# Kernel optimization log

Hardware: AMD Instinct MI355X
Metric: run time of the kernel (lower is better)

The kernel has to match this reference:

```python
import jax, jax.numpy as jnp
import numpy as np

N_NODES = 100000
N_EDGES = 1600000
D_IN = 128
D_OUT = 128


def setup_inputs() -> dict:
    key = jax.random.key(0)
    ks = jax.random.split(key, 7)
    x = jax.random.normal(ks[0], (N_NODES, D_IN), dtype=jnp.float32)
    y = jax.random.normal(ks[1], (N_NODES, D_OUT), dtype=jnp.float32)
    edge_src = jax.random.randint(ks[2], (N_EDGES,), 0, N_NODES, dtype=jnp.int32)
    edge_dst = jax.random.randint(ks[3], (N_EDGES,), 0, N_NODES, dtype=jnp.int32)
    adj_vals = jax.random.uniform(ks[4], (N_EDGES,), dtype=jnp.float32)
    weight = jax.random.normal(ks[5], (D_IN, D_OUT), dtype=jnp.float32) * (1.0 / np.sqrt(D_IN))
    bias = jax.random.normal(ks[6], (D_OUT,), dtype=jnp.float32) * 0.01
    return {"x": x, "y": y, "edge_src": edge_src, "edge_dst": edge_dst,
            "adj_vals": adj_vals, "weight": weight, "bias": bias}


def reference(x, y, edge_src, edge_dst, adj_vals, weight, bias):
    # GraphConvolution: support = x @ W ; out = spmm(adj, support) + bias
    support = x @ weight                      # [N, d_out]
    msgs = support[edge_src] * adj_vals[:, None]   # [E, d_out] gather + scale
    agg = jax.ops.segment_sum(msgs, edge_dst, num_segments=N_NODES)  # [N, d_out]
    gc_out = agg + bias
    # ResGCN epilogue: relu(gc_out + y); dropout is identity in eval (p=0.0)
    return jax.nn.relu(gc_out + y)
```

## Files before the change

kernel.cpp:

```cpp
#include <hip/hip_runtime.h>

#define D 128
#define CE 8192
#define NB_MAX 1024
#define MAXC 512
#define EBUF 3072
#define CHUNK 1024
#define WTP 136


typedef __attribute__((ext_vector_type(8))) short bf16x8;
typedef __attribute__((ext_vector_type(4))) float f32x4;

__device__ __forceinline__ unsigned short f2bf(float f) {
  unsigned u = __float_as_uint(f);
  unsigned r = (u + 0x7fffu + ((u >> 16) & 1u)) >> 16;
  return (unsigned short)r;
}

__device__ __forceinline__ int wave_iscan(int v) {
  const int lane = threadIdx.x & 63;
#pragma unroll
  for (int off = 1; off < 64; off <<= 1) {
    int u = __shfl_up(v, off, 64);
    if (lane >= off) v += u;
  }
  return v;
}

__device__ __forceinline__ int seg_find(const int* pref, int nC, int i) {
  int lo = 0, hi = nC;
  while (hi - lo > 1) {
    int mid = (lo + hi) >> 1;
    if (pref[mid] <= i) lo = mid; else hi = mid;
  }
  return lo;
}

__global__ __launch_bounds__(256) void convert_kernel(
    const float4* __restrict__ x4, ushort4* __restrict__ xb4, int n4, int nxblk,
    const float* __restrict__ w, unsigned short* __restrict__ wt) {
  int bid = blockIdx.x;
  if (bid < nxblk) {
    int i = bid * 256 + threadIdx.x;
    if (i < n4) {
      float4 v = x4[i];
      ushort4 r;
      r.x = f2bf(v.x);
      r.y = f2bf(v.y);
      r.z = f2bf(v.z);
      r.w = f2bf(v.w);
      xb4[i] = r;
    }
  } else {
    int idx = (bid - nxblk) * 256 + threadIdx.x;
    int n = idx >> 7, k = idx & 127;
    wt[n * WTP + k] = f2bf(w[k * D + n]);
  }
}

__global__ __launch_bounds__(1024) void chunk_sort_kernel(
    const int* __restrict__ src, const int* __restrict__ dst,
    const float* __restrict__ adj, int2* __restrict__ edges,
    unsigned short* __restrict__ ofs, int nE, int nB) {
  __shared__ int2 stage[CE];
  __shared__ int h[NB_MAX + 4];
  __shared__ int wsum[16];
  const int t = threadIdx.x;
  const int c = blockIdx.x;
  const int e0 = c * CE;
  const int n = min(CE, nE - e0);
  const int lane = t & 63, wid = t >> 6;

  for (int i = t; i < NB_MAX + 4; i += 1024) h[i] = 0;
  __syncthreads();

  int dreg[8];
#pragma unroll
  for (int k = 0; k < 8; ++k) {
    int i = k * 1024 + t;
    if (i < n) {
      int d = dst[e0 + i];
      dreg[k] = d;
      atomicAdd(&h[d >> 7], 1);
    }
  }
  __syncthreads();

  int v = h[t];
  int inc = wave_iscan(v);
  if (lane == 63) wsum[wid] = inc;
  __syncthreads();
  if (wid == 0) {
    int p = (lane < 16) ? wsum[lane] : 0;
    int pi = wave_iscan(p);
    if (lane < 16) wsum[lane] = pi;
  }
  __syncthreads();
  h[t] = inc - v + (wid ? wsum[wid - 1] : 0);
  __syncthreads();

  unsigned short* o = ofs + (size_t)c * (nB + 1);
  for (int i = t; i <= nB; i += 1024)
    o[i] = (unsigned short)(i < NB_MAX ? h[i] : n);
  __syncthreads();

#pragma unroll
  for (int k = 0; k < 8; ++k) {
    int i = k * 1024 + t;
    if (i < n) {
      int d = dreg[k];
      int pos = atomicAdd(&h[d >> 7], 1);
      int2 ev;
      ev.x = src[e0 + i] | ((d & 127) << 17);
      ev.y = __float_as_int(adj[e0 + i]);
      stage[pos] = ev;
    }
  }
  __syncthreads();

  for (int i = t; i < n; i += 1024) edges[e0 + i] = stage[i];
}

__global__ __launch_bounds__(256) void bucket_gather_kernel(
    const int2* __restrict__ tmp, const unsigned short* __restrict__ ofs,
    const uint2* __restrict__ xb, char* out, int nC, int nB, int nNodes) {
  __shared__ int2 ebuf[EBUF];
  __shared__ int segst[MAXC];
  __shared__ int pref[MAXC + 1];
  __shared__ int cnt[128];
  __shared__ int cur[128];
  __shared__ int sstart[128];
  __shared__ int w4[4];
  const int t = threadIdx.x;
  const int b = blockIdx.x;
  const int lane = t & 63, wid = t >> 6;

  const int c0 = 2 * t, c1 = 2 * t + 1;
  int n0 = 0, n1 = 0;
  if (c0 < nC) {
    int s0 = ofs[(size_t)c0 * (nB + 1) + b];
    int s1 = ofs[(size_t)c0 * (nB + 1) + b + 1];
    segst[c0] = c0 * CE + s0;
    n0 = s1 - s0;
  }
  if (c1 < nC) {
    int s0 = ofs[(size_t)c1 * (nB + 1) + b];
    int s1 = ofs[(size_t)c1 * (nB + 1) + b + 1];
    segst[c1] = c1 * CE + s0;
    n1 = s1 - s0;
  }
  int tt = n0 + n1;
  int inc = wave_iscan(tt);
  if (lane == 63) w4[wid] = inc;
  __syncthreads();
  int add = 0;
  for (int i = 0; i < wid; ++i) add += w4[i];
  int incl = inc + add;
  int excl = incl - tt;
  if (c0 < nC) pref[c0] = excl;
  if (c1 < nC) pref[c1] = excl + n0;
  if (t == 255) pref[nC] = incl;
  __syncthreads();
  const int m = pref[nC];

  const int gi = t >> 5;
  const int q = t & 31;
  float4 acc[16];
#pragma unroll
  for (int k = 0; k < 16; ++k) acc[k] = make_float4(0.f, 0.f, 0.f, 0.f);

  for (int w0 = 0; w0 < m; w0 += EBUF) {
    const int w1 = min(m, w0 + EBUF);
    if (t < 128) cnt[t] = 0;
    __syncthreads();

    for (int i = w0 + t; i < w1; i += 256) {
      int lo = seg_find(pref, nC, i);
      int sx = ((const int*)tmp)[(size_t)(segst[lo] + (i - pref[lo])) * 2];
      atomicAdd(&cnt[(sx >> 17) & 127], 1);
    }
    __syncthreads();

    int cv = (t < 128) ? cnt[t] : 0;
    int cinc = wave_iscan(cv);
    if (t == 63) w4[0] = cinc;
    __syncthreads();
    int cst = cinc - cv + ((t >= 64 && t < 128) ? w4[0] : 0);
    if (t < 128) {
      sstart[t] = cst;
      cur[t] = cst;
    }
    __syncthreads();

    for (int i = w0 + t; i < w1; i += 256) {
      int lo = seg_find(pref, nC, i);
      int2 ev = tmp[segst[lo] + (i - pref[lo])];
      int pos = atomicAdd(&cur[(ev.x >> 17) & 127], 1);
      ebuf[pos] = ev;
    }
    __syncthreads();

#pragma unroll
    for (int k = 0; k < 16; ++k) {
      const int dl = gi * 16 + k;
      int j = sstart[dl];
      const int e = cur[dl];
      for (; j + 3 < e; j += 4) {
        int2 e0 = ebuf[j], e1 = ebuf[j + 1], e2 = ebuf[j + 2], e3 = ebuf[j + 3];
        float a0 = __int_as_float(e0.y), a1 = __int_as_float(e1.y);
        float a2 = __int_as_float(e2.y), a3 = __int_as_float(e3.y);
        uint2 v0 = xb[(size_t)(e0.x & 0x1FFFF) * 32 + q];
        uint2 v1 = xb[(size_t)(e1.x & 0x1FFFF) * 32 + q];
        uint2 v2 = xb[(size_t)(e2.x & 0x1FFFF) * 32 + q];
        uint2 v3 = xb[(size_t)(e3.x & 0x1FFFF) * 32 + q];
        acc[k].x = fmaf(a0, __uint_as_float(v0.x << 16), acc[k].x);
        acc[k].y = fmaf(a0, __uint_as_float(v0.x & 0xffff0000u), acc[k].y);
        acc[k].z = fmaf(a0, __uint_as_float(v0.y << 16), acc[k].z);
        acc[k].w = fmaf(a0, __uint_as_float(v0.y & 0xffff0000u), acc[k].w);
        acc[k].x = fmaf(a1, __uint_as_float(v1.x << 16), acc[k].x);
        acc[k].y = fmaf(a1, __uint_as_float(v1.x & 0xffff0000u), acc[k].y);
        acc[k].z = fmaf(a1, __uint_as_float(v1.y << 16), acc[k].z);
        acc[k].w = fmaf(a1, __uint_as_float(v1.y & 0xffff0000u), acc[k].w);
        acc[k].x = fmaf(a2, __uint_as_float(v2.x << 16), acc[k].x);
        acc[k].y = fmaf(a2, __uint_as_float(v2.x & 0xffff0000u), acc[k].y);
        acc[k].z = fmaf(a2, __uint_as_float(v2.y << 16), acc[k].z);
        acc[k].w = fmaf(a2, __uint_as_float(v2.y & 0xffff0000u), acc[k].w);
        acc[k].x = fmaf(a3, __uint_as_float(v3.x << 16), acc[k].x);
        acc[k].y = fmaf(a3, __uint_as_float(v3.x & 0xffff0000u), acc[k].y);
        acc[k].z = fmaf(a3, __uint_as_float(v3.y << 16), acc[k].z);
        acc[k].w = fmaf(a3, __uint_as_float(v3.y & 0xffff0000u), acc[k].w);
      }
      for (; j < e; ++j) {
        int2 e0 = ebuf[j];
        float a0 = __int_as_float(e0.y);
        uint2 v0 = xb[(size_t)(e0.x & 0x1FFFF) * 32 + q];
        acc[k].x = fmaf(a0, __uint_as_float(v0.x << 16), acc[k].x);
        acc[k].y = fmaf(a0, __uint_as_float(v0.x & 0xffff0000u), acc[k].y);
        acc[k].z = fmaf(a0, __uint_as_float(v0.y << 16), acc[k].z);
        acc[k].w = fmaf(a0, __uint_as_float(v0.y & 0xffff0000u), acc[k].w);
      }
    }
    __syncthreads();
  }

#pragma unroll
  for (int k = 0; k < 16; ++k) {
    int g = b * 128 + gi * 16 + k;
    if (g < nNodes) {
      uint2 pk;
      pk.x = (unsigned)f2bf(acc[k].x) | ((unsigned)f2bf(acc[k].y) << 16);
      pk.y = (unsigned)f2bf(acc[k].z) | ((unsigned)f2bf(acc[k].w) << 16);
      ((uint2*)(out + (size_t)g * 512))[q] = pk;
    }
  }
}

__global__ __launch_bounds__(256) void gemm_mfma_kernel(
    const char* aggb, const unsigned short* __restrict__ wt,
    const float* __restrict__ y, const float* __restrict__ bias,
    float* out, int nNodes) {
  __shared__ unsigned short sWt[D * WTP];
  const int t = threadIdx.x;
  for (int i = t; i < D * WTP / 8; i += 256)
    ((int4*)sWt)[i] = ((const int4*)wt)[i];
  __syncthreads();

  const int w = t >> 6, l = t & 63;
  const int quad = l >> 4, m = l & 15;
  const int row0 = blockIdx.x * 128 + w * 32;

  const int ar0 = min(row0 + m, nNodes - 1);
  const int ar1 = min(row0 + 16 + m, nNodes - 1);
  const char* pa0 = aggb + (size_t)ar0 * 512;
  const char* pa1 = aggb + (size_t)ar1 * 512;

  f32x4 acc0[8], acc1[8];
#pragma unroll
  for (int nt = 0; nt < 8; ++nt) {
    acc0[nt] = (f32x4){0.f, 0.f, 0.f, 0.f};
    acc1[nt] = (f32x4){0.f, 0.f, 0.f, 0.f};
  }

#pragma unroll
  for (int ks = 0; ks < 4; ++ks) {
    const int kof = ks * 32 + quad * 8;
    bf16x8 a0 = *(const bf16x8*)(pa0 + kof * 2);
    bf16x8 a1 = *(const bf16x8*)(pa1 + kof * 2);
#pragma unroll
    for (int nt = 0; nt < 8; ++nt) {
      bf16x8 b = *(const bf16x8*)&sWt[(nt * 16 + m) * WTP + kof];
      acc0[nt] = __builtin_amdgcn_mfma_f32_16x16x32_bf16(a0, b, acc0[nt], 0, 0, 0);
      acc1[nt] = __builtin_amdgcn_mfma_f32_16x16x32_bf16(a1, b, acc1[nt], 0, 0, 0);
    }
  }

  float bv[8];
#pragma unroll
  for (int nt = 0; nt < 8; ++nt) bv[nt] = bias[nt * 16 + m];

#pragma unroll
  for (int s = 0; s < 2; ++s) {
#pragma unroll
    for (int r = 0; r < 4; ++r) {
      int row = row0 + s * 16 + quad * 4 + r;
      if (row >= nNodes) continue;
      const float* yr = y + (size_t)row * D;
      float* orow = out + (size_t)row * D;
#pragma unroll
      for (int nt = 0; nt < 8; ++nt) {
        int c = nt * 16 + m;
        float v = (s == 0 ? acc0[nt][r] : acc1[nt][r]) + yr[c] + bv[nt];
        orow[c] = fmaxf(v, 0.f);
      }
    }
  }
}

__global__ __launch_bounds__(256) void zero_counts_kernel(int* __restrict__ c, int n) {
  int i = blockIdx.x * 256 + threadIdx.x;
  if (i < n) c[i] = 0;
}

__global__ __launch_bounds__(256) void hist_kernel(
    const int* __restrict__ dst, int* __restrict__ counts, int nE) {
  int e = blockIdx.x * 256 + threadIdx.x;
  if (e < nE) atomicAdd(&counts[dst[e]], 1);
}

__global__ __launch_bounds__(256) void scan_partial_kernel(
    const int* __restrict__ counts, int* __restrict__ chunk_sum, int n) {
  __shared__ int sdata[256];
  int b = blockIdx.x, t = threadIdx.x;
  int base = b * CHUNK + t * 4;
  int s = 0;
#pragma unroll
  for (int k = 0; k < 4; ++k) {
    int i = base + k;
    if (i < n) s += counts[i];
  }
  sdata[t] = s;
  __syncthreads();
  for (int off = 128; off > 0; off >>= 1) {
    if (t < off) sdata[t] += sdata[t + off];
    __syncthreads();
  }
  if (t == 0) chunk_sum[b] = sdata[0];
}

__global__ void scan_chunks_kernel(const int* __restrict__ chunk_sum,
                                   int* __restrict__ chunk_off,
                                   int* __restrict__ row_start, int nchunks, int n) {
  if (threadIdx.x == 0 && blockIdx.x == 0) {
    int run = 0;
    for (int i = 0; i < nchunks; ++i) {
      chunk_off[i] = run;
      run += chunk_sum[i];
    }
    row_start[n] = run;
  }
}

__global__ __launch_bounds__(256) void scan_final_kernel(
    const int* __restrict__ counts, const int* __restrict__ chunk_off,
    int* __restrict__ row_start, int* __restrict__ cursor, int n) {
  __shared__ int sdata[256];
  int b = blockIdx.x, t = threadIdx.x;
  int base = b * CHUNK + t * 4;
  int c[4] = {0, 0, 0, 0};
#pragma unroll
  for (int k = 0; k < 4; ++k) {
    int i = base + k;
    if (i < n) c[k] = counts[i];
  }
  int tsum = c[0] + c[1] + c[2] + c[3];
  sdata[t] = tsum;
  __syncthreads();
  for (int off = 1; off < 256; off <<= 1) {
    int v = (t >= off) ? sdata[t - off] : 0;
    __syncthreads();
    sdata[t] += v;
    __syncthreads();
  }
  int run = sdata[t] - tsum + chunk_off[b];
#pragma unroll
  for (int k = 0; k < 4; ++k) {
    int i = base + k;
    if (i < n) {
      row_start[i] = run;
      cursor[i] = run;
      run += c[k];
    }
  }
}

__global__ __launch_bounds__(256) void scatter_sort_kernel(
    const int* __restrict__ src, const int* __restrict__ dst,
    const float* __restrict__ adj, int* __restrict__ cursor,
    int2* __restrict__ edges, int nE) {
  int e = blockIdx.x * 256 + threadIdx.x;
  if (e >= nE) return;
  int d = dst[e];
  int2 ev;
  ev.x = src[e];
  ev.y = __float_as_int(adj[e]);
  int pos = atomicAdd(&cursor[d], 1);
  edges[pos] = ev;
}

__global__ __launch_bounds__(256) void gather_fp32_kernel(
    const float* __restrict__ x, const int* __restrict__ row_start,
    const int2* __restrict__ edges, float* __restrict__ out, int nNodes) {
  int g = (blockIdx.x * 256 + threadIdx.x) >> 5;
  int q = threadIdx.x & 31;
  if (g >= nNodes) return;
  int beg = row_start[g], end = row_start[g + 1];
  const float4* x4 = (const float4*)x;
  float4 acc = make_float4(0.f, 0.f, 0.f, 0.f);
  for (int j = beg; j < end; ++j) {
    int2 e0 = edges[j];
    float a0 = __int_as_float(e0.y);
    float4 v0 = x4[(size_t)e0.x * 32 + q];
    acc.x = fmaf(a0, v0.x, acc.x);
    acc.y = fmaf(a0, v0.y, acc.y);
    acc.z = fmaf(a0, v0.z, acc.z);
    acc.w = fmaf(a0, v0.w, acc.w);
  }
  ((float4*)out)[(size_t)g * 32 + q] = acc;
}

__global__ __launch_bounds__(256) void zero_kernel(float4* __restrict__ out, int n4) {
  int i = blockIdx.x * 256 + threadIdx.x;
  if (i < n4) out[i] = make_float4(0.f, 0.f, 0.f, 0.f);
}

__global__ __launch_bounds__(256) void scatter_atomic_kernel(
    const float* __restrict__ x, const int* __restrict__ src,
    const int* __restrict__ dst, const float* __restrict__ adj,
    float* __restrict__ out, int nE) {
  int tid = blockIdx.x * 256 + threadIdx.x;
  int e = tid >> 5;
  int q = tid & 31;
  if (e >= nE) return;
  int s = src[e];
  int d = dst[e];
  float a = adj[e];
  float4 v = ((const float4*)x)[(size_t)s * 32 + q];
  float* o = out + (size_t)d * D + q * 4;
  atomicAdd(o + 0, v.x * a);
  atomicAdd(o + 1, v.y * a);
  atomicAdd(o + 2, v.z * a);
  atomicAdd(o + 3, v.w * a);
}

__global__ __launch_bounds__(256) void gemm_fused_kernel(
    float* __restrict__ out, const float* __restrict__ w,
    const float* __restrict__ y, const float* __restrict__ bias, int nrows) {
  __shared__ float sW[D * D];
  __shared__ float sA[32 * D];
  const int tid = threadIdx.x;
  const int row0 = blockIdx.x * 32;

  const float4* w4 = (const float4*)w;
  float4* sW4 = (float4*)sW;
  for (int i = tid; i < D * D / 4; i += 256) sW4[i] = w4[i];

  const int nrow_blk = min(32, nrows - row0);
  const float4* out4_base = (const float4*)(out + (size_t)row0 * D);
  float4* sA4 = (float4*)sA;
  for (int i = tid; i < nrow_blk * 32; i += 256) sA4[i] = out4_base[i];
  __syncthreads();

  const int cg = tid & 31;
  const int rs = tid >> 5;

  float4 acc[4];
#pragma unroll
  for (int r = 0; r < 4; ++r) acc[r] = make_float4(0.f, 0.f, 0.f, 0.f);

#pragma unroll 4
  for (int k4 = 0; k4 < 32; ++k4) {
    float4 wv0 = sW4[(k4 * 4 + 0) * 32 + cg];
    float4 wv1 = sW4[(k4 * 4 + 1) * 32 + cg];
    float4 wv2 = sW4[(k4 * 4 + 2) * 32 + cg];
    float4 wv3 = sW4[(k4 * 4 + 3) * 32 + cg];
#pragma unroll
    for (int r = 0; r < 4; ++r) {
      float4 xv = sA4[(rs + r * 8) * 32 + k4];
      acc[r].x = fmaf(xv.x, wv0.x, acc[r].x);
      acc[r].y = fmaf(xv.x, wv0.y, acc[r].y);
      acc[r].z = fmaf(xv.x, wv0.z, acc[r].z);
      acc[r].w = fmaf(xv.x, wv0.w, acc[r].w);
      acc[r].x = fmaf(xv.y, wv1.x, acc[r].x);
      acc[r].y = fmaf(xv.y, wv1.y, acc[r].y);
      acc[r].z = fmaf(xv.y, wv1.z, acc[r].z);
      acc[r].w = fmaf(xv.y, wv1.w, acc[r].w);
      acc[r].x = fmaf(xv.z, wv2.x, acc[r].x);
      acc[r].y = fmaf(xv.z, wv2.y, acc[r].y);
      acc[r].z = fmaf(xv.z, wv2.z, acc[r].z);
      acc[r].w = fmaf(xv.z, wv2.w, acc[r].w);
      acc[r].x = fmaf(xv.w, wv3.x, acc[r].x);
      acc[r].y = fmaf(xv.w, wv3.y, acc[r].y);
      acc[r].z = fmaf(xv.w, wv3.z, acc[r].z);
      acc[r].w = fmaf(xv.w, wv3.w, acc[r].w);
    }
  }

  const float4* y4 = (const float4*)y;
  const float4* b4 = (const float4*)bias;
  float4* o4 = (float4*)out;
  float4 bv = b4[cg];
#pragma unroll
  for (int r = 0; r < 4; ++r) {
    int row = row0 + rs + r * 8;
    if (row < nrows) {
      float4 yv = y4[(size_t)row * 32 + cg];
      float4 res;
      res.x = fmaxf(acc[r].x + yv.x + bv.x, 0.f);
      res.y = fmaxf(acc[r].y + yv.y + bv.y, 0.f);
      res.z = fmaxf(acc[r].z + yv.z + bv.z, 0.f);
      res.w = fmaxf(acc[r].w + yv.w + bv.w, 0.f);
      o4[(size_t)row * 32 + cg] = res;
    }
  }
}

extern "C" void kernel_launch(void* const* d_in, const int* in_sizes, int n_in,
                              void* d_out, int out_size, void* d_ws, size_t ws_size,
                              hipStream_t stream) {
  const float* x    = (const float*)d_in[0];
  const float* y    = (const float*)d_in[1];
  const int*   esrc = (const int*)d_in[2];
  const int*   edst = (const int*)d_in[3];
  const float* adj  = (const float*)d_in[4];
  const float* w    = (const float*)d_in[5];
  const float* bias = (const float*)d_in[6];
  float* out = (float*)d_out;

  const int nNodes = in_sizes[0] / D;
  const int nE = in_sizes[2];
  const int n4 = nNodes * (D / 4);
  const int nB = (nNodes + 127) >> 7;
  const int nC = (nE + CE - 1) / CE;

  const size_t ofs_bytes = (((size_t)nC * (nB + 1) * 2) + 15) & ~(size_t)15;
  const size_t wt_bytes  = (size_t)D * WTP * 2;
  const size_t tmp_bytes = (size_t)nC * CE * 8;
  const size_t xb_bytes  = (size_t)nNodes * D * 2;
  const size_t need1 = ofs_bytes + wt_bytes + tmp_bytes + xb_bytes;

  const int nchunks = (nNodes + CHUNK - 1) / CHUNK;
  const size_t e2_bytes  = (size_t)nE * 8;
  const size_t int_bytes = (size_t)(3 * nNodes + 1 + 2 * nchunks) * 4;
  const size_t need2 = e2_bytes + int_bytes;

  if (ws_size >= need1 && nNodes <= NB_MAX * 128 && nC <= MAXC) {
    char* p = (char*)d_ws;
    unsigned short* ofs = (unsigned short*)p;   p += ofs_bytes;
    unsigned short* wt = (unsigned short*)p;    p += wt_bytes;
    int2* tmp = (int2*)p;                       p += tmp_bytes;
    ushort4* xb4 = (ushort4*)p;

    const int nxblk = (n4 + 255) / 256;
    chunk_sort_kernel<<<nC, 1024, 0, stream>>>(esrc, edst, adj, tmp, ofs, nE, nB);
    convert_kernel<<<nxblk + 64, 256, 0, stream>>>((const float4*)x, xb4, n4,
                                                   nxblk, w, wt);
    bucket_gather_kernel<<<nB, 256, 0, stream>>>(
        tmp, ofs, (const uint2*)xb4, (char*)d_out, nC, nB, nNodes);
    gemm_mfma_kernel<<<(nNodes + 127) / 128, 256, 0, stream>>>(
        (const char*)d_out, wt, y, bias, out, nNodes);
  } else if (ws_size >= need2) {
    char* base = (char*)d_ws;
    int2* edges = (int2*)base;
    int* counts = (int*)(base + e2_bytes);
    int* row_start = counts + nNodes;
    int* cursor = row_start + nNodes + 1;
    int* chunk_sum = cursor + nNodes;
    int* chunk_off = chunk_sum + nchunks;

    zero_counts_kernel<<<(nNodes + 255) / 256, 256, 0, stream>>>(counts, nNodes);
    hist_kernel<<<(nE + 255) / 256, 256, 0, stream>>>(edst, counts, nE);
    scan_partial_kernel<<<nchunks, 256, 0, stream>>>(counts, chunk_sum, nNodes);
    scan_chunks_kernel<<<1, 64, 0, stream>>>(chunk_sum, chunk_off, row_start,
                                             nchunks, nNodes);
    scan_final_kernel<<<nchunks, 256, 0, stream>>>(counts, chunk_off, row_start,
                                                   cursor, nNodes);
    scatter_sort_kernel<<<(nE + 255) / 256, 256, 0, stream>>>(
        esrc, edst, adj, cursor, edges, nE);
    gather_fp32_kernel<<<(nNodes * 32 + 255) / 256, 256, 0, stream>>>(
        x, row_start, edges, out, nNodes);
    gemm_fused_kernel<<<(nNodes + 31) / 32, 256, 0, stream>>>(out, w, y, bias,
                                                              nNodes);
  } else {
    zero_kernel<<<(n4 + 255) / 256, 256, 0, stream>>>((float4*)out, n4);
    scatter_atomic_kernel<<<((size_t)nE * 32 + 255) / 256, 256, 0, stream>>>(
        x, esrc, edst, adj, out, nE);
    gemm_fused_kernel<<<(nNodes + 31) / 32, 256, 0, stream>>>(out, w, y, bias,
                                                              nNodes);
  }
}
```

Before: 305.1 us.

## Halve sort chunk size and double gather threads per destination bucket

Sort chunks shrink from 8192 to 4096 edges and the sort kernel drops to 512 threads, so twice as many sort blocks run in parallel. The bucket gather kernel grows to 512 threads, with each 32-lane group owning 8 destination rows instead of 16, one chunk per thread in the segment scan. The aim is more parallelism and occupancy in the gather phase and fewer accumulator registers per thread. In exchange, every gather block now has twice as many segments to read offsets for and to binary-search over, and the per-chunk offset table doubles in size.

```diff
diff --git a/kernel.cpp b/kernel.cpp
--- a/kernel.cpp
+++ b/kernel.cpp
@@ -1,7 +1,7 @@
 #include <hip/hip_runtime.h>
 
 #define D 128
-#define CE 8192
+#define CE 4096
 #define NB_MAX 1024
 #define MAXC 512
 #define EBUF 3072
@@ -59,26 +59,26 @@
   }
 }
 
-__global__ __launch_bounds__(1024) void chunk_sort_kernel(
+__global__ __launch_bounds__(512) void chunk_sort_kernel(
     const int* __restrict__ src, const int* __restrict__ dst,
     const float* __restrict__ adj, int2* __restrict__ edges,
     unsigned short* __restrict__ ofs, int nE, int nB) {
   __shared__ int2 stage[CE];
   __shared__ int h[NB_MAX + 4];
-  __shared__ int wsum[16];
+  __shared__ int wsum[8];
   const int t = threadIdx.x;
   const int c = blockIdx.x;
   const int e0 = c * CE;
   const int n = min(CE, nE - e0);
   const int lane = t & 63, wid = t >> 6;
 
-  for (int i = t; i < NB_MAX + 4; i += 1024) h[i] = 0;
+  for (int i = t; i < NB_MAX + 4; i += 512) h[i] = 0;
   __syncthreads();
 
   int dreg[8];
 #pragma unroll
   for (int k = 0; k < 8; ++k) {
-    int i = k * 1024 + t;
+    int i = k * 512 + t;
     if (i < n) {
       int d = dst[e0 + i];
       dreg[k] = d;
@@ -87,27 +87,26 @@
   }
   __syncthreads();
 
-  int v = h[t];
-  int inc = wave_iscan(v);
+  int v0 = h[2 * t], v1 = h[2 * t + 1];
+  int tt = v0 + v1;
+  int inc = wave_iscan(tt);
   if (lane == 63) wsum[wid] = inc;
   __syncthreads();
-  if (wid == 0) {
-    int p = (lane < 16) ? wsum[lane] : 0;
-    int pi = wave_iscan(p);
-    if (lane < 16) wsum[lane] = pi;
-  }
-  __syncthreads();
-  h[t] = inc - v + (wid ? wsum[wid - 1] : 0);
+  int add = 0;
+  for (int i = 0; i < wid; ++i) add += wsum[i];
+  int excl = inc + add - tt;
+  h[2 * t] = excl;
+  h[2 * t + 1] = excl + v0;
   __syncthreads();
 
   unsigned short* o = ofs + (size_t)c * (nB + 1);
-  for (int i = t; i <= nB; i += 1024)
+  for (int i = t; i <= nB; i += 512)
     o[i] = (unsigned short)(i < NB_MAX ? h[i] : n);
   __syncthreads();
 
 #pragma unroll
   for (int k = 0; k < 8; ++k) {
-    int i = k * 1024 + t;
+    int i = k * 512 + t;
     if (i < n) {
       int d = dreg[k];
       int pos = atomicAdd(&h[d >> 7], 1);
@@ -119,10 +118,10 @@
   }
   __syncthreads();
 
-  for (int i = t; i < n; i += 1024) edges[e0 + i] = stage[i];
-}
-
-__global__ __launch_bounds__(256) void bucket_gather_kernel(
+  for (int i = t; i < n; i += 512) edges[e0 + i] = stage[i];
+}
+
+__global__ __launch_bounds__(512) void bucket_gather_kernel(
     const int2* __restrict__ tmp, const unsigned short* __restrict__ ofs,
     const uint2* __restrict__ xb, char* out, int nC, int nB, int nNodes) {
   __shared__ int2 ebuf[EBUF];
@@ -131,51 +130,41 @@
   __shared__ int cnt[128];
   __shared__ int cur[128];
   __shared__ int sstart[128];
-  __shared__ int w4[4];
+  __shared__ int w8[8];
   const int t = threadIdx.x;
   const int b = blockIdx.x;
   const int lane = t & 63, wid = t >> 6;
 
-  const int c0 = 2 * t, c1 = 2 * t + 1;
-  int n0 = 0, n1 = 0;
-  if (c0 < nC) {
-    int s0 = ofs[(size_t)c0 * (nB + 1) + b];
-    int s1 = ofs[(size_t)c0 * (nB + 1) + b + 1];
-    segst[c0] = c0 * CE + s0;
-    n0 = s1 - s0;
-  }
-  if (c1 < nC) {
-    int s0 = ofs[(size_t)c1 * (nB + 1) + b];
-    int s1 = ofs[(size_t)c1 * (nB + 1) + b + 1];
-    segst[c1] = c1 * CE + s0;
-    n1 = s1 - s0;
-  }
-  int tt = n0 + n1;
+  int tt = 0;
+  if (t < nC) {
+    int s0 = ofs[(size_t)t * (nB + 1) + b];
+    int s1 = ofs[(size_t)t * (nB + 1) + b + 1];
+    segst[t] = t * CE + s0;
+    tt = s1 - s0;
+  }
   int inc = wave_iscan(tt);
-  if (lane == 63) w4[wid] = inc;
+  if (lane == 63) w8[wid] = inc;
   __syncthreads();
   int add = 0;
-  for (int i = 0; i < wid; ++i) add += w4[i];
+  for (int i = 0; i < wid; ++i) add += w8[i];
   int incl = inc + add;
-  int excl = incl - tt;
-  if (c0 < nC) pref[c0] = excl;
-  if (c1 < nC) pref[c1] = excl + n0;
-  if (t == 255) pref[nC] = incl;
+  if (t < nC) pref[t] = incl - tt;
+  if (t == nC - 1) pref[nC] = incl;
   __syncthreads();
   const int m = pref[nC];
 
   const int gi = t >> 5;
   const int q = t & 31;
-  float4 acc[16];
-#pragma unroll
-  for (int k = 0; k < 16; ++k) acc[k] = make_float4(0.f, 0.f, 0.f, 0.f);
+  float4 acc[8];
+#pragma unroll
+  for (int k = 0; k < 8; ++k) acc[k] = make_float4(0.f, 0.f, 0.f, 0.f);
 
   for (int w0 = 0; w0 < m; w0 += EBUF) {
     const int w1 = min(m, w0 + EBUF);
     if (t < 128) cnt[t] = 0;
     __syncthreads();
 
-    for (int i = w0 + t; i < w1; i += 256) {
+    for (int i = w0 + t; i < w1; i += 512) {
       int lo = seg_find(pref, nC, i);
       int sx = ((const int*)tmp)[(size_t)(segst[lo] + (i - pref[lo])) * 2];
       atomicAdd(&cnt[(sx >> 17) & 127], 1);
@@ -184,16 +173,16 @@
 
     int cv = (t < 128) ? cnt[t] : 0;
     int cinc = wave_iscan(cv);
-    if (t == 63) w4[0] = cinc;
-    __syncthreads();
-    int cst = cinc - cv + ((t >= 64 && t < 128) ? w4[0] : 0);
+    if (t == 63) w8[0] = cinc;
+    __syncthreads();
+    int cst = cinc - cv + ((t >= 64 && t < 128) ? w8[0] : 0);
     if (t < 128) {
       sstart[t] = cst;
       cur[t] = cst;
     }
     __syncthreads();
 
-    for (int i = w0 + t; i < w1; i += 256) {
+    for (int i = w0 + t; i < w1; i += 512) {
       int lo = seg_find(pref, nC, i);
       int2 ev = tmp[segst[lo] + (i - pref[lo])];
       int pos = atomicAdd(&cur[(ev.x >> 17) & 127], 1);
@@ -202,8 +191,8 @@
     __syncthreads();
 
 #pragma unroll
-    for (int k = 0; k < 16; ++k) {
-      const int dl = gi * 16 + k;
+    for (int k = 0; k < 8; ++k) {
+      const int dl = gi * 8 + k;
       int j = sstart[dl];
       const int e = cur[dl];
       for (; j + 3 < e; j += 4) {
@@ -245,8 +234,8 @@
   }
 
 #pragma unroll
-  for (int k = 0; k < 16; ++k) {
-    int g = b * 128 + gi * 16 + k;
+  for (int k = 0; k < 8; ++k) {
+    int g = b * 128 + gi * 8 + k;
     if (g < nNodes) {
       uint2 pk;
       pk.x = (unsigned)f2bf(acc[k].x) | ((unsigned)f2bf(acc[k].y) << 16);
@@ -562,10 +551,10 @@
     ushort4* xb4 = (ushort4*)p;
 
     const int nxblk = (n4 + 255) / 256;
-    chunk_sort_kernel<<<nC, 1024, 0, stream>>>(esrc, edst, adj, tmp, ofs, nE, nB);
+    chunk_sort_kernel<<<nC, 512, 0, stream>>>(esrc, edst, adj, tmp, ofs, nE, nB);
     convert_kernel<<<nxblk + 64, 256, 0, stream>>>((const float4*)x, xb4, n4,
                                                    nxblk, w, wt);
-    bucket_gather_kernel<<<nB, 256, 0, stream>>>(
+    bucket_gather_kernel<<<nB, 512, 0, stream>>>(
         tmp, ofs, (const uint2*)xb4, (char*)d_out, nC, nB, nNodes);
     gemm_mfma_kernel<<<(nNodes + 127) / 128, 256, 0, stream>>>(
         (const char*)d_out, wt, y, bias, out, nNodes);
```

Measured after the change: 352.4 us. +15.5%, slower.

## Split each bucket across two blocks and unroll gather loop by eight

Applied to the files above, without the earlier changes.

The bucket gather kernel now launches two blocks per 128-node bucket. Each block handles 64 destination nodes and filters the bucket's edges by half, which halves the accumulator registers and doubles the block count, giving more parallelism and occupancy. The inner gather loop is also unrolled to eight edges so more global loads are in flight at once. In exchange, each block still scans and seg-finds the whole bucket's edge list, so reads of the staged edges and the prefix setup work are doubled.

```diff
diff --git a/kernel.cpp b/kernel.cpp
--- a/kernel.cpp
+++ b/kernel.cpp
@@ -128,12 +128,13 @@
   __shared__ int2 ebuf[EBUF];
   __shared__ int segst[MAXC];
   __shared__ int pref[MAXC + 1];
-  __shared__ int cnt[128];
-  __shared__ int cur[128];
-  __shared__ int sstart[128];
+  __shared__ int cnt[64];
+  __shared__ int cur[64];
+  __shared__ int sstart[64];
   __shared__ int w4[4];
   const int t = threadIdx.x;
-  const int b = blockIdx.x;
+  const int b = blockIdx.x >> 1;
+  const int p = blockIdx.x & 1;
   const int lane = t & 63, wid = t >> 6;
 
   const int c0 = 2 * t, c1 = 2 * t + 1;
@@ -166,54 +167,64 @@
 
   const int gi = t >> 5;
   const int q = t & 31;
-  float4 acc[16];
-#pragma unroll
-  for (int k = 0; k < 16; ++k) acc[k] = make_float4(0.f, 0.f, 0.f, 0.f);
+  float4 acc[8];
+#pragma unroll
+  for (int k = 0; k < 8; ++k) acc[k] = make_float4(0.f, 0.f, 0.f, 0.f);
 
   for (int w0 = 0; w0 < m; w0 += EBUF) {
     const int w1 = min(m, w0 + EBUF);
-    if (t < 128) cnt[t] = 0;
+    if (t < 64) cnt[t] = 0;
     __syncthreads();
 
     for (int i = w0 + t; i < w1; i += 256) {
       int lo = seg_find(pref, nC, i);
       int sx = ((const int*)tmp)[(size_t)(segst[lo] + (i - pref[lo])) * 2];
-      atomicAdd(&cnt[(sx >> 17) & 127], 1);
-    }
-    __syncthreads();
-
-    int cv = (t < 128) ? cnt[t] : 0;
+      int dl = (sx >> 17) & 127;
+      if ((dl >> 6) == p) atomicAdd(&cnt[dl & 63], 1);
+    }
+    __syncthreads();
+
+    int cv = (t < 64) ? cnt[t] : 0;
     int cinc = wave_iscan(cv);
-    if (t == 63) w4[0] = cinc;
-    __syncthreads();
-    int cst = cinc - cv + ((t >= 64 && t < 128) ? w4[0] : 0);
-    if (t < 128) {
-      sstart[t] = cst;
-      cur[t] = cst;
+    if (t < 64) {
+      sstart[t] = cinc - cv;
+      cur[t] = cinc - cv;
     }
     __syncthreads();
 
     for (int i = w0 + t; i < w1; i += 256) {
       int lo = seg_find(pref, nC, i);
       int2 ev = tmp[segst[lo] + (i - pref[lo])];
-      int pos = atomicAdd(&cur[(ev.x >> 17) & 127], 1);
-      ebuf[pos] = ev;
-    }
-    __syncthreads();
-
-#pragma unroll
-    for (int k = 0; k < 16; ++k) {
-      const int dl = gi * 16 + k;
+      int dl = (ev.x >> 17) & 127;
+      if ((dl >> 6) == p) {
+        int pos = atomicAdd(&cur[dl & 63], 1);
+        ebuf[pos] = ev;
+      }
+    }
+    __syncthreads();
+
+#pragma unroll
+    for (int k = 0; k < 8; ++k) {
+      const int dl = gi * 8 + k;
       int j = sstart[dl];
       const int e = cur[dl];
-      for (; j + 3 < e; j += 4) {
-        int2 e0 = ebuf[j], e1 = ebuf[j + 1], e2 = ebuf[j + 2], e3 = ebuf[j + 3];
-        float a0 = __int_as_float(e0.y), a1 = __int_as_float(e1.y);
-        float a2 = __int_as_float(e2.y), a3 = __int_as_float(e3.y);
-        uint2 v0 = xb[(size_t)(e0.x & 0x1FFFF) * 32 + q];
-        uint2 v1 = xb[(size_t)(e1.x & 0x1FFFF) * 32 + q];
-        uint2 v2 = xb[(size_t)(e2.x & 0x1FFFF) * 32 + q];
-        uint2 v3 = xb[(size_t)(e3.x & 0x1FFFF) * 32 + q];
+      for (; j + 7 < e; j += 8) {
+        int2 ee0 = ebuf[j + 0], ee1 = ebuf[j + 1];
+        int2 ee2 = ebuf[j + 2], ee3 = ebuf[j + 3];
+        int2 ee4 = ebuf[j + 4], ee5 = ebuf[j + 5];
+        int2 ee6 = ebuf[j + 6], ee7 = ebuf[j + 7];
+        uint2 v0 = xb[(size_t)(ee0.x & 0x1FFFF) * 32 + q];
+        uint2 v1 = xb[(size_t)(ee1.x & 0x1FFFF) * 32 + q];
+        uint2 v2 = xb[(size_t)(ee2.x & 0x1FFFF) * 32 + q];
+        uint2 v3 = xb[(size_t)(ee3.x & 0x1FFFF) * 32 + q];
+        uint2 v4 = xb[(size_t)(ee4.x & 0x1FFFF) * 32 + q];
+        uint2 v5 = xb[(size_t)(ee5.x & 0x1FFFF) * 32 + q];
+        uint2 v6 = xb[(size_t)(ee6.x & 0x1FFFF) * 32 + q];
+        uint2 v7 = xb[(size_t)(ee7.x & 0x1FFFF) * 32 + q];
+        float a0 = __int_as_float(ee0.y), a1 = __int_as_float(ee1.y);
+        float a2 = __int_as_float(ee2.y), a3 = __int_as_float(ee3.y);
+        float a4 = __int_as_float(ee4.y), a5 = __int_as_float(ee5.y);
+        float a6 = __int_as_float(ee6.y), a7 = __int_as_float(ee7.y);
         acc[k].x = fmaf(a0, __uint_as_float(v0.x << 16), acc[k].x);
         acc[k].y = fmaf(a0, __uint_as_float(v0.x & 0xffff0000u), acc[k].y);
         acc[k].z = fmaf(a0, __uint_as_float(v0.y << 16), acc[k].z);
@@ -230,6 +241,22 @@
         acc[k].y = fmaf(a3, __uint_as_float(v3.x & 0xffff0000u), acc[k].y);
         acc[k].z = fmaf(a3, __uint_as_float(v3.y << 16), acc[k].z);
         acc[k].w = fmaf(a3, __uint_as_float(v3.y & 0xffff0000u), acc[k].w);
+        acc[k].x = fmaf(a4, __uint_as_float(v4.x << 16), acc[k].x);
+        acc[k].y = fmaf(a4, __uint_as_float(v4.x & 0xffff0000u), acc[k].y);
+        acc[k].z = fmaf(a4, __uint_as_float(v4.y << 16), acc[k].z);
+        acc[k].w = fmaf(a4, __uint_as_float(v4.y & 0xffff0000u), acc[k].w);
+        acc[k].x = fmaf(a5, __uint_as_float(v5.x << 16), acc[k].x);
+        acc[k].y = fmaf(a5, __uint_as_float(v5.x & 0xffff0000u), acc[k].y);
+        acc[k].z = fmaf(a5, __uint_as_float(v5.y << 16), acc[k].z);
+        acc[k].w = fmaf(a5, __uint_as_float(v5.y & 0xffff0000u), acc[k].w);
+        acc[k].x = fmaf(a6, __uint_as_float(v6.x << 16), acc[k].x);
+        acc[k].y = fmaf(a6, __uint_as_float(v6.x & 0xffff0000u), acc[k].y);
+        acc[k].z = fmaf(a6, __uint_as_float(v6.y << 16), acc[k].z);
+        acc[k].w = fmaf(a6, __uint_as_float(v6.y & 0xffff0000u), acc[k].w);
+        acc[k].x = fmaf(a7, __uint_as_float(v7.x << 16), acc[k].x);
+        acc[k].y = fmaf(a7, __uint_as_float(v7.x & 0xffff0000u), acc[k].y);
+        acc[k].z = fmaf(a7, __uint_as_float(v7.y << 16), acc[k].z);
+        acc[k].w = fmaf(a7, __uint_as_float(v7.y & 0xffff0000u), acc[k].w);
       }
       for (; j < e; ++j) {
         int2 e0 = ebuf[j];
@@ -245,8 +272,8 @@
   }
 
 #pragma unroll
-  for (int k = 0; k < 16; ++k) {
-    int g = b * 128 + gi * 16 + k;
+  for (int k = 0; k < 8; ++k) {
+    int g = b * 128 + p * 64 + gi * 8 + k;
     if (g < nNodes) {
       uint2 pk;
       pk.x = (unsigned)f2bf(acc[k].x) | ((unsigned)f2bf(acc[k].y) << 16);
@@ -565,7 +592,7 @@
     chunk_sort_kernel<<<nC, 1024, 0, stream>>>(esrc, edst, adj, tmp, ofs, nE, nB);
     convert_kernel<<<nxblk + 64, 256, 0, stream>>>((const float4*)x, xb4, n4,
                                                    nxblk, w, wt);
-    bucket_gather_kernel<<<nB, 256, 0, stream>>>(
+    bucket_gather_kernel<<<nB * 2, 256, 0, stream>>>(
         tmp, ofs, (const uint2*)xb4, (char*)d_out, nC, nB, nNodes);
     gemm_mfma_kernel<<<(nNodes + 127) / 128, 256, 0, stream>>>(
         (const char*)d_out, wt, y, bias, out, nNodes);
```

Result: slower. 335.6 us (+10.0%).

## Fuse bucket gather aggregation with MFMA GEMM epilogue via shared memory

Applied to the files above, without the earlier changes.

The gather kernel now keeps each 128-row block's aggregated bf16 rows in shared memory and runs the MFMA projection plus the bias, residual and ReLU epilogue in the same kernel. This removes the separate GEMM launch and the global round trip of the intermediate aggregate buffer. Weight tiles are read directly from global memory (relying on cache) rather than staged in LDS. The added ~35KB shared buffer raises LDS use per block and may reduce occupancy of the gather phase.

```diff
diff --git a/kernel.cpp b/kernel.cpp
--- a/kernel.cpp
+++ b/kernel.cpp
@@ -122,10 +122,13 @@
   for (int i = t; i < n; i += 1024) edges[e0 + i] = stage[i];
 }
 
-__global__ __launch_bounds__(256) void bucket_gather_kernel(
+__global__ __launch_bounds__(256) void bucket_fused_kernel(
     const int2* __restrict__ tmp, const unsigned short* __restrict__ ofs,
-    const uint2* __restrict__ xb, char* out, int nC, int nB, int nNodes) {
+    const uint2* __restrict__ xb, const unsigned short* __restrict__ wt,
+    const float* __restrict__ y, const float* __restrict__ bias,
+    float* __restrict__ out, int nC, int nB, int nNodes) {
   __shared__ int2 ebuf[EBUF];
+  __shared__ unsigned short agg[128 * WTP];
   __shared__ int segst[MAXC];
   __shared__ int pref[MAXC + 1];
   __shared__ int cnt[128];
@@ -246,34 +249,19 @@
 
 #pragma unroll
   for (int k = 0; k < 16; ++k) {
-    int g = b * 128 + gi * 16 + k;
-    if (g < nNodes) {
-      uint2 pk;
-      pk.x = (unsigned)f2bf(acc[k].x) | ((unsigned)f2bf(acc[k].y) << 16);
-      pk.y = (unsigned)f2bf(acc[k].z) | ((unsigned)f2bf(acc[k].w) << 16);
-      ((uint2*)(out + (size_t)g * 512))[q] = pk;
-    }
-  }
-}
-
-__global__ __launch_bounds__(256) void gemm_mfma_kernel(
-    const char* aggb, const unsigned short* __restrict__ wt,
-    const float* __restrict__ y, const float* __restrict__ bias,
-    float* out, int nNodes) {
-  __shared__ unsigned short sWt[D * WTP];
-  const int t = threadIdx.x;
-  for (int i = t; i < D * WTP / 8; i += 256)
-    ((int4*)sWt)[i] = ((const int4*)wt)[i];
+    const int dl = gi * 16 + k;
+    uint2 pk;
+    pk.x = (unsigned)f2bf(acc[k].x) | ((unsigned)f2bf(acc[k].y) << 16);
+    pk.y = (unsigned)f2bf(acc[k].z) | ((unsigned)f2bf(acc[k].w) << 16);
+    *(uint2*)&agg[dl * WTP + q * 4] = pk;
+  }
   __syncthreads();
 
   const int w = t >> 6, l = t & 63;
-  const int quad = l >> 4, m = l & 15;
-  const int row0 = blockIdx.x * 128 + w * 32;
-
-  const int ar0 = min(row0 + m, nNodes - 1);
-  const int ar1 = min(row0 + 16 + m, nNodes - 1);
-  const char* pa0 = aggb + (size_t)ar0 * 512;
-  const char* pa1 = aggb + (size_t)ar1 * 512;
+  const int quad = l >> 4, mm = l & 15;
+  const int row0 = b * 128 + w * 32;
+  const char* pa0 = (const char*)&agg[(w * 32 + mm) * WTP];
+  const char* pa1 = (const char*)&agg[(w * 32 + 16 + mm) * WTP];
 
   f32x4 acc0[8], acc1[8];
 #pragma unroll
@@ -289,15 +277,15 @@
     bf16x8 a1 = *(const bf16x8*)(pa1 + kof * 2);
 #pragma unroll
     for (int nt = 0; nt < 8; ++nt) {
-      bf16x8 b = *(const bf16x8*)&sWt[(nt * 16 + m) * WTP + kof];
-      acc0[nt] = __builtin_amdgcn_mfma_f32_16x16x32_bf16(a0, b, acc0[nt], 0, 0, 0);
-      acc1[nt] = __builtin_amdgcn_mfma_f32_16x16x32_bf16(a1, b, acc1[nt], 0, 0, 0);
+      bf16x8 bb = *(const bf16x8*)&wt[(nt * 16 + mm) * WTP + kof];
+      acc0[nt] = __builtin_amdgcn_mfma_f32_16x16x32_bf16(a0, bb, acc0[nt], 0, 0, 0);
+      acc1[nt] = __builtin_amdgcn_mfma_f32_16x16x32_bf16(a1, bb, acc1[nt], 0, 0, 0);
     }
   }
 
   float bv[8];
 #pragma unroll
-  for (int nt = 0; nt < 8; ++nt) bv[nt] = bias[nt * 16 + m];
+  for (int nt = 0; nt < 8; ++nt) bv[nt] = bias[nt * 16 + mm];
 
 #pragma unroll
   for (int s = 0; s < 2; ++s) {
@@ -309,7 +297,7 @@
       float* orow = out + (size_t)row * D;
 #pragma unroll
       for (int nt = 0; nt < 8; ++nt) {
-        int c = nt * 16 + m;
+        int c = nt * 16 + mm;
         float v = (s == 0 ? acc0[nt][r] : acc1[nt][r]) + yr[c] + bv[nt];
         orow[c] = fmaxf(v, 0.f);
       }
@@ -565,10 +553,8 @@
     chunk_sort_kernel<<<nC, 1024, 0, stream>>>(esrc, edst, adj, tmp, ofs, nE, nB);
     convert_kernel<<<nxblk + 64, 256, 0, stream>>>((const float4*)x, xb4, n4,
                                                    nxblk, w, wt);
-    bucket_gather_kernel<<<nB, 256, 0, stream>>>(
-        tmp, ofs, (const uint2*)xb4, (char*)d_out, nC, nB, nNodes);
-    gemm_mfma_kernel<<<(nNodes + 127) / 128, 256, 0, stream>>>(
-        (const char*)d_out, wt, y, bias, out, nNodes);
+    bucket_fused_kernel<<<nB, 256, 0, stream>>>(
+        tmp, ofs, (const uint2*)xb4, wt, y, bias, out, nC, nB, nNodes);
   } else if (ws_size >= need2) {
     char* base = (char*)d_ws;
     int2* edges = (int2*)base;
```

Result: no change. 310.1 us (+1.6%).
